# Optimization experiments

Hardware: AMD Instinct MI355X
Metric: run time of the kernel (lower is better)

## Reference

```python
import jax, jax.numpy as jnp
import numpy as np

N, C, T, V, S = 64, 64, 300, 25, 3  # batch, channels, frames, joints, num_subset
EPS_NORM = 1e-4  # L2_norm epsilon from the torch module
EPS_BN = 1e-5    # torch BatchNorm2d default eps


def setup_inputs() -> dict:
    key = jax.random.key(0)
    ks = jax.random.split(key, 6)
    x = jax.random.normal(ks[0], (N, C, T, V), jnp.float32)
    # adaptive adjacency PA: (num_subset, V, V)
    PA = jax.random.normal(ks[1], (S, V, V), jnp.float32)
    # per-subset 1x1 conv: weight (out_c, in_c), bias (out_c,); conv_branch_init scale
    W = jax.random.normal(ks[2], (S, C, C), jnp.float32) * np.sqrt(2.0 / (C * S)).astype(np.float32)
    b = jax.random.normal(ks[3], (S, C), jnp.float32) * 0.01
    # BatchNorm affine params (training-mode batch stats used in forward)
    gamma = 1.0 + 0.1 * jax.random.normal(ks[4], (C,), jnp.float32)
    beta = 0.1 * jax.random.normal(ks[5], (C,), jnp.float32)
    return {"x": x, "PA": PA, "W": W, "b": b, "gamma": gamma, "beta": beta}


def reference(x, PA, W, b, gamma, beta):
    # L2 normalize adjacency along dim=1 (per subset, per column)
    A = PA / (jnp.linalg.norm(PA, axis=1, keepdims=True) + EPS_NORM)  # (S, V, V)
    # sum over subsets of: graph matmul (nctv,vw->nctw) then 1x1 conv (oc contraction)
    y = jnp.einsum('nctv,svw,soc->notw', x, A, W)
    y = y + b.sum(axis=0)[None, :, None, None]
    # BatchNorm2d in training mode: batch stats over (N, T, V) per channel
    mean = y.mean(axis=(0, 2, 3), keepdims=True)
    var = y.var(axis=(0, 2, 3), keepdims=True)  # biased variance
    y = gamma[None, :, None, None] * (y - mean) * jax.lax.rsqrt(var + EPS_BN) + beta[None, :, None, None]
    # residual (in_c == out_c -> down is identity) + ReLU
    return jax.nn.relu(y + x)
```

## Files before the change

### kernel.cpp

```cpp
#include <hip/hip_runtime.h>
#include <math.h>


typedef __attribute__((ext_vector_type(8))) short bf16x8;
typedef __attribute__((ext_vector_type(4))) float f32x4;
typedef __attribute__((ext_vector_type(4))) ushort u16x4;
typedef __attribute__((ext_vector_type(8))) ushort u16x8;

__device__ inline ushort f2bf(float f) {
    union { float f; unsigned u; } v; v.f = f;
    unsigned r = v.u + 0x7fffu + ((v.u >> 16) & 1u);
    return (ushort)(r >> 16);
}
__device__ inline float bf2f(ushort h) {
    union { unsigned u; float f; } v; v.u = ((unsigned)h) << 16;
    return v.f;
}

__global__ __launch_bounds__(256) void k_prep(const float* __restrict__ PA,
                                              const float* __restrict__ W,
                                              float* __restrict__ ws) {
    __shared__ float Al[1875];
    const int tid = threadIdx.x;
    const int bid = blockIdx.x;
    for (int i = tid; i < 1875; i += 256) Al[i] = PA[i];
    if (bid == 0)
        for (int i = tid; i < 2048; i += 256) ws[2048 + i] = 0.0f;
    __syncthreads();
    if (tid < 75) {
        int s = tid / 25, w = tid - s * 25;
        float ss = 0.0f;
        for (int v = 0; v < 25; ++v) {
            float p = Al[s * 625 + v * 25 + w];
            ss += p * p;
        }
        float inv = 1.0f / (sqrtf(ss) + 1e-4f);
        for (int v = 0; v < 25; ++v) Al[s * 625 + v * 25 + w] *= inv;
    }
    __syncthreads();
    int idx = bid * 256 + tid;
    if (idx < 1536) {
        ushort* wt = (ushort*)(ws + 4352);
        int lane = idx & 63, rest = idx >> 6;
        int wv = rest & 3, sk = rest >> 2;
        int kt = sk & 1, s = sk >> 1;
        int col = lane & 15, quad = lane >> 4;
        const float* wp = W + s * 4096 + (wv * 16 + col) * 64 + kt * 32 + quad * 8;
#pragma unroll
        for (int j = 0; j < 8; ++j) wt[idx * 8 + j] = f2bf(wp[j]);
    } else if (idx < 1920) {
        ushort* at = (ushort*)(ws + 10496);
        int a = idx - 1536;
        int lane = a & 63, rest = a >> 6;
        int nt2 = rest & 1, s = rest >> 1;
        int col = lane & 15, quad = lane >> 4;
        int w = nt2 * 16 + col;
#pragma unroll
        for (int j = 0; j < 8; ++j) {
            int v = quad * 4 + (j < 4 ? j : j + 12);
            float av = (v < 25 && w < 25) ? Al[s * 625 + v * 25 + w] : 0.0f;
            at[a * 8 + j] = f2bf(av);
        }
    }
}

__global__ __launch_bounds__(256, 3) void k_main15(const float* __restrict__ x,
                                                   const float* __restrict__ ws,
                                                   ushort* __restrict__ ypre,
                                                   float* __restrict__ stats) {
    __shared__ __align__(16) ushort Xl[112 * 72];
    __shared__ float sst[128];

    const int tid = threadIdx.x;
    const int wv = tid >> 6;
    const int lane = tid & 63;
    const int col = lane & 15;
    const int quad = lane >> 4;
    const int strip = wv << 4;
    const int n = blockIdx.y;
    const int bx = blockIdx.x;
    const int t0 = bx * 4;

    const ushort* wt = (const ushort*)(ws + 4352);
    const ushort* at = (const ushort*)(ws + 10496);

    bf16x8 wf[6], af[6];
#pragma unroll
    for (int s = 0; s < 3; ++s) {
        wf[s * 2 + 0] = *(const bf16x8*)&wt[(((s * 2 + 0) * 4 + wv) * 64 + lane) * 8];
        wf[s * 2 + 1] = *(const bf16x8*)&wt[(((s * 2 + 1) * 4 + wv) * 64 + lane) * 8];
        af[s * 2 + 0] = *(const bf16x8*)&at[((s * 2 + 0) * 64 + lane) * 8];
        af[s * 2 + 1] = *(const bf16x8*)&at[((s * 2 + 1) * 64 + lane) * 8];
    }

    {
        const float* xr = x + n * 480000 + t0 * 25;
        const int c = tid >> 2, part = tid & 3;
        const float4* row = (const float4*)(xr + c * 7500);
        for (int j = part; j < 25; j += 4) {
            float4 v4 = row[j];
            ushort* dst = &Xl[(j * 4) * 72 + c];
            dst[0]   = f2bf(v4.x);
            dst[72]  = f2bf(v4.y);
            dst[144] = f2bf(v4.z);
            dst[216] = f2bf(v4.w);
        }
        for (int i = tid; i < 864; i += 256) Xl[7200 + i] = 0;
    }
    __syncthreads();

    f32x4 yacc[4][2];
#pragma unroll
    for (int t = 0; t < 4; ++t)
#pragma unroll
        for (int j = 0; j < 2; ++j) yacc[t][j] = (f32x4){0.f, 0.f, 0.f, 0.f};

#pragma unroll
    for (int s = 0; s < 3; ++s) {
#pragma unroll
        for (int t = 0; t < 4; ++t) {
            const int r0 = (t * 25 + col) * 72 + (quad << 3);
            const int r1 = r0 + 16 * 72;
            bf16x8 x00 = *(const bf16x8*)&Xl[r0];
            bf16x8 x01 = *(const bf16x8*)&Xl[r0 + 32];
            bf16x8 x10 = *(const bf16x8*)&Xl[r1];
            bf16x8 x11 = *(const bf16x8*)&Xl[r1 + 32];
            f32x4 zA = (f32x4){0.f, 0.f, 0.f, 0.f};
            f32x4 zB = (f32x4){0.f, 0.f, 0.f, 0.f};
            zA = __builtin_amdgcn_mfma_f32_16x16x32_bf16(x00, wf[s * 2 + 0], zA, 0, 0, 0);
            zA = __builtin_amdgcn_mfma_f32_16x16x32_bf16(x01, wf[s * 2 + 1], zA, 0, 0, 0);
            zB = __builtin_amdgcn_mfma_f32_16x16x32_bf16(x10, wf[s * 2 + 0], zB, 0, 0, 0);
            zB = __builtin_amdgcn_mfma_f32_16x16x32_bf16(x11, wf[s * 2 + 1], zB, 0, 0, 0);
            union { unsigned u[4]; bf16x8 v; } zf;
            zf.u[0] = (unsigned)f2bf(zA[0]) | ((unsigned)f2bf(zA[1]) << 16);
            zf.u[1] = (unsigned)f2bf(zA[2]) | ((unsigned)f2bf(zA[3]) << 16);
            zf.u[2] = (unsigned)f2bf(zB[0]) | ((unsigned)f2bf(zB[1]) << 16);
            zf.u[3] = (unsigned)f2bf(zB[2]) | ((unsigned)f2bf(zB[3]) << 16);
            yacc[t][0] = __builtin_amdgcn_mfma_f32_16x16x32_bf16(zf.v, af[s * 2 + 0], yacc[t][0], 0, 0, 0);
            yacc[t][1] = __builtin_amdgcn_mfma_f32_16x16x32_bf16(zf.v, af[s * 2 + 1], yacc[t][1], 0, 0, 0);
        }
    }

    __syncthreads();
    ushort* Ys = Xl;

    float ssum[4] = {0.f, 0.f, 0.f, 0.f}, ssq[4] = {0.f, 0.f, 0.f, 0.f};
    const int obase = strip + (quad << 2);
#pragma unroll
    for (int t = 0; t < 4; ++t)
#pragma unroll
        for (int nt2 = 0; nt2 < 2; ++nt2) {
            int w = nt2 * 16 + col;
            if (w < 25) {
                f32x4 f = yacc[t][nt2];
#pragma unroll
                for (int r = 0; r < 4; ++r) {
                    float yv = f[r];
                    Ys[(obase + r) * 100 + t * 25 + w] = f2bf(yv);
                    ssum[r] += yv;
                    ssq[r] = fmaf(yv, yv, ssq[r]);
                }
            }
        }
#pragma unroll
    for (int r = 0; r < 4; ++r) {
        float a = ssum[r], b = ssq[r];
        for (int m = 1; m < 16; m <<= 1) {
            a += __shfl_xor(a, m, 64);
            b += __shfl_xor(b, m, 64);
        }
        if (col == 0) {
            sst[obase + r] = a;
            sst[64 + obase + r] = b;
        }
    }
    __syncthreads();
    {
        u16x8* dst = (u16x8*)(ypre + (size_t)(n * 75 + bx) * 6400);
        const u16x8* src = (const u16x8*)Ys;
        for (int i = tid; i < 800; i += 256) dst[i] = src[i];
    }
    const int rep = (bx + blockIdx.y) & 15;
    if (tid < 128) atomicAdd(&stats[rep * 128 + tid], sst[tid]);
}

__global__ __launch_bounds__(256) void k_bnrelu_d(const float* __restrict__ x,
                                                  const ushort* __restrict__ ypre,
                                                  const float* __restrict__ stats,
                                                  const float* __restrict__ gamma,
                                                  const float* __restrict__ beta,
                                                  float* __restrict__ out) {
    __shared__ float bsc[2];
    const int plane = blockIdx.x;
    const int o = plane & 63;
    const int n = plane >> 6;
    const int tid = threadIdx.x;
    if (tid < 16) {
        float su = stats[tid * 128 + o];
        float sq = stats[tid * 128 + 64 + o];
#pragma unroll
        for (int m = 1; m < 16; m <<= 1) {
            su += __shfl_xor(su, m, 64);
            sq += __shfl_xor(sq, m, 64);
        }
        if (tid == 0) {
            const float invn = 1.0f / 480000.0f;
            float mean = su * invn;
            float var = sq * invn - mean * mean;
            float sc = gamma[o] * rsqrtf(var + 1e-5f);
            bsc[0] = sc;
            bsc[1] = beta[o] - mean * sc;
        }
    }
    __syncthreads();
    const float sc = bsc[0], sh = bsc[1];
    const ushort* ybase = ypre + (size_t)n * 480000 + o * 100;
    const f32x4* xp = (const f32x4*)(x + (size_t)plane * 7500);
    f32x4* op = (f32x4*)(out + (size_t)plane * 7500);
    for (int j4 = tid; j4 < 1875; j4 += 256) {
        int bxi = j4 / 25;
        int r4 = j4 - bxi * 25;
        u16x4 yv = *(const u16x4*)(ybase + bxi * 6400 + r4 * 4);
        f32x4 xx = xp[j4];
        f32x4 r;
        r.x = fmaxf(fmaf(bf2f(yv.x), sc, sh) + xx.x, 0.0f);
        r.y = fmaxf(fmaf(bf2f(yv.y), sc, sh) + xx.y, 0.0f);
        r.z = fmaxf(fmaf(bf2f(yv.z), sc, sh) + xx.z, 0.0f);
        r.w = fmaxf(fmaf(bf2f(yv.w), sc, sh) + xx.w, 0.0f);
        __builtin_nontemporal_store(r, &op[j4]);
    }
}

extern "C" void kernel_launch(void* const* d_in, const int* in_sizes, int n_in,
                              void* d_out, int out_size, void* d_ws, size_t ws_size,
                              hipStream_t stream) {
    const float* x = (const float*)d_in[0];
    const float* PA = (const float*)d_in[1];
    const float* W = (const float*)d_in[2];
    const float* gamma = (const float*)d_in[4];
    const float* beta = (const float*)d_in[5];
    float* wsf = (float*)d_ws;
    float* out = (float*)d_out;
    ushort* ypre = (ushort*)((char*)d_ws + 65536);

    k_prep<<<8, 256, 0, stream>>>(PA, W, wsf);
    dim3 g(75, 64);
    k_main15<<<g, 256, 0, stream>>>(x, wsf, ypre, wsf + 2048);
    k_bnrelu_d<<<4096, 256, 0, stream>>>(x, ypre, wsf + 2048, gamma, beta, out);
}
```

Baseline: 292.2 us.

## Process six frames per block and store ypre in natural NCTV layout

```diff
diff --git a/kernel.cpp b/kernel.cpp
--- a/kernel.cpp
+++ b/kernel.cpp
@@ -5,7 +5,6 @@
 typedef __attribute__((ext_vector_type(8))) short bf16x8;
 typedef __attribute__((ext_vector_type(4))) float f32x4;
 typedef __attribute__((ext_vector_type(4))) ushort u16x4;
-typedef __attribute__((ext_vector_type(8))) ushort u16x8;
 
 __device__ inline ushort f2bf(float f) {
     union { float f; unsigned u; } v; v.f = f;
@@ -64,11 +63,11 @@
     }
 }
 
-__global__ __launch_bounds__(256, 3) void k_main15(const float* __restrict__ x,
+__global__ __launch_bounds__(256, 3) void k_main16(const float* __restrict__ x,
                                                    const float* __restrict__ ws,
                                                    ushort* __restrict__ ypre,
                                                    float* __restrict__ stats) {
-    __shared__ __align__(16) ushort Xl[112 * 72];
+    __shared__ __align__(16) ushort Xl[160 * 72];
     __shared__ float sst[128];
 
     const int tid = threadIdx.x;
@@ -79,7 +78,6 @@
     const int strip = wv << 4;
     const int n = blockIdx.y;
     const int bx = blockIdx.x;
-    const int t0 = bx * 4;
 
     const ushort* wt = (const ushort*)(ws + 4352);
     const ushort* at = (const ushort*)(ws + 10496);
@@ -94,10 +92,10 @@
     }
 
     {
-        const float* xr = x + n * 480000 + t0 * 25;
+        const float* xr = x + n * 480000 + bx * 150;
         const int c = tid >> 2, part = tid & 3;
         const float4* row = (const float4*)(xr + c * 7500);
-        for (int j = part; j < 25; j += 4) {
+        for (int j = part; j < 37; j += 4) {
             float4 v4 = row[j];
             ushort* dst = &Xl[(j * 4) * 72 + c];
             dst[0]   = f2bf(v4.x);
@@ -105,20 +103,25 @@
             dst[144] = f2bf(v4.z);
             dst[216] = f2bf(v4.w);
         }
-        for (int i = tid; i < 864; i += 256) Xl[7200 + i] = 0;
-    }
-    __syncthreads();
-
-    f32x4 yacc[4][2];
-#pragma unroll
-    for (int t = 0; t < 4; ++t)
+        if (tid < 64) {
+            float2 v2 = *(const float2*)(xr + tid * 7500 + 148);
+            Xl[148 * 72 + tid] = f2bf(v2.x);
+            Xl[149 * 72 + tid] = f2bf(v2.y);
+        }
+        for (int i = tid; i < 720; i += 256) Xl[10800 + i] = 0;
+    }
+    __syncthreads();
+
+    f32x4 yacc[6][2];
+#pragma unroll
+    for (int t = 0; t < 6; ++t)
 #pragma unroll
         for (int j = 0; j < 2; ++j) yacc[t][j] = (f32x4){0.f, 0.f, 0.f, 0.f};
 
 #pragma unroll
     for (int s = 0; s < 3; ++s) {
 #pragma unroll
-        for (int t = 0; t < 4; ++t) {
+        for (int t = 0; t < 6; ++t) {
             const int r0 = (t * 25 + col) * 72 + (quad << 3);
             const int r1 = r0 + 16 * 72;
             bf16x8 x00 = *(const bf16x8*)&Xl[r0];
@@ -147,7 +150,7 @@
     float ssum[4] = {0.f, 0.f, 0.f, 0.f}, ssq[4] = {0.f, 0.f, 0.f, 0.f};
     const int obase = strip + (quad << 2);
 #pragma unroll
-    for (int t = 0; t < 4; ++t)
+    for (int t = 0; t < 6; ++t)
 #pragma unroll
         for (int nt2 = 0; nt2 < 2; ++nt2) {
             int w = nt2 * 16 + col;
@@ -156,7 +159,7 @@
 #pragma unroll
                 for (int r = 0; r < 4; ++r) {
                     float yv = f[r];
-                    Ys[(obase + r) * 100 + t * 25 + w] = f2bf(yv);
+                    Ys[(obase + r) * 150 + t * 25 + w] = f2bf(yv);
                     ssum[r] += yv;
                     ssq[r] = fmaf(yv, yv, ssq[r]);
                 }
@@ -176,15 +179,20 @@
     }
     __syncthreads();
     {
-        u16x8* dst = (u16x8*)(ypre + (size_t)(n * 75 + bx) * 6400);
-        const u16x8* src = (const u16x8*)Ys;
-        for (int i = tid; i < 800; i += 256) dst[i] = src[i];
+        const unsigned* src = (const unsigned*)Ys;
+        for (int idx = lane; idx < 1200; idx += 64) {
+            int oo = idx / 75;
+            int r2 = idx - oo * 75;
+            int o = strip + oo;
+            *(unsigned*)(ypre + (size_t)n * 480000 + o * 7500 + bx * 150 + r2 * 2) =
+                src[o * 75 + r2];
+        }
     }
     const int rep = (bx + blockIdx.y) & 15;
     if (tid < 128) atomicAdd(&stats[rep * 128 + tid], sst[tid]);
 }
 
-__global__ __launch_bounds__(256) void k_bnrelu_d(const float* __restrict__ x,
+__global__ __launch_bounds__(256) void k_bnrelu_f(const float* __restrict__ x,
                                                   const ushort* __restrict__ ypre,
                                                   const float* __restrict__ stats,
                                                   const float* __restrict__ gamma,
@@ -193,7 +201,6 @@
     __shared__ float bsc[2];
     const int plane = blockIdx.x;
     const int o = plane & 63;
-    const int n = plane >> 6;
     const int tid = threadIdx.x;
     if (tid < 16) {
         float su = stats[tid * 128 + o];
@@ -214,13 +221,11 @@
     }
     __syncthreads();
     const float sc = bsc[0], sh = bsc[1];
-    const ushort* ybase = ypre + (size_t)n * 480000 + o * 100;
+    const u16x4* yp = (const u16x4*)(ypre + (size_t)plane * 7500);
     const f32x4* xp = (const f32x4*)(x + (size_t)plane * 7500);
     f32x4* op = (f32x4*)(out + (size_t)plane * 7500);
     for (int j4 = tid; j4 < 1875; j4 += 256) {
-        int bxi = j4 / 25;
-        int r4 = j4 - bxi * 25;
-        u16x4 yv = *(const u16x4*)(ybase + bxi * 6400 + r4 * 4);
+        u16x4 yv = yp[j4];
         f32x4 xx = xp[j4];
         f32x4 r;
         r.x = fmaxf(fmaf(bf2f(yv.x), sc, sh) + xx.x, 0.0f);
@@ -244,7 +249,7 @@
     ushort* ypre = (ushort*)((char*)d_ws + 65536);
 
     k_prep<<<8, 256, 0, stream>>>(PA, W, wsf);
-    dim3 g(75, 64);
-    k_main15<<<g, 256, 0, stream>>>(x, wsf, ypre, wsf + 2048);
-    k_bnrelu_d<<<4096, 256, 0, stream>>>(x, ypre, wsf + 2048, gamma, beta, out);
-}
+    dim3 g(50, 64);
+    k_main16<<<g, 256, 0, stream>>>(x, wsf, ypre, wsf + 2048);
+    k_bnrelu_f<<<4096, 256, 0, stream>>>(x, ypre, wsf + 2048, gamma, beta, out);
+}
```

New measurement: 376.5 us. 1.29x slower.
